# Kernel optimization log

Hardware: AMD Instinct MI355X
Metric: run time of the kernel (lower is better)

## Reference

```python
import jax, jax.numpy as jnp
import numpy as np

B, S, F = 4, 2048, 8
D, H, L, FF = 256, 8, 2, 1024
DH = D // H
NSK, NPAT = 2000, 64
DQ = D // 4  # pattern/feat sub-embedding width


def setup_inputs() -> dict:
    key = jax.random.key(0)
    ks = jax.random.split(key, 32)
    r = lambda i, shape: jax.random.normal(ks[i], shape, jnp.float32) * 0.02
    return {
        'interactions': jax.random.randint(ks[0], (B, S), 0, 2 * NSK),
        'patterns': jax.random.randint(ks[1], (B, S), 0, NPAT),
        'forget_features': jax.random.normal(ks[2], (B, S, F), jnp.float32),
        'inter_emb': r(3, (2 * NSK, D)),
        'pattern_emb': r(4, (NPAT, DQ)),
        'feat_W': r(5, (F, DQ)), 'feat_b': jnp.zeros((DQ,), jnp.float32),
        'in_W': r(6, (D + 2 * DQ, D)), 'in_b': jnp.zeros((D,), jnp.float32),
        'time_W': r(7, (1, D)), 'time_b': jnp.zeros((D,), jnp.float32),
        'pos_W': r(8, (1, D)), 'pos_b': jnp.zeros((D,), jnp.float32),
        'Wq': r(9, (L, D, H, DH)), 'bq': jnp.zeros((L, H, DH), jnp.float32),
        'Wk': r(10, (L, D, H, DH)), 'bk': jnp.zeros((L, H, DH), jnp.float32),
        'Wv': r(11, (L, D, H, DH)), 'bv': jnp.zeros((L, H, DH), jnp.float32),
        'Wo': r(12, (L, H, DH, D)), 'bo': jnp.zeros((L, D), jnp.float32),
        'kerple_p': jnp.full((L, H, 1, 1), 0.5, jnp.float32),
        'kerple_a': jnp.zeros((L, H, 1, 1), jnp.float32),
        'ln1_g': jnp.ones((L, D), jnp.float32), 'ln1_b': jnp.zeros((L, D), jnp.float32),
        'ln2_g': jnp.ones((L, D), jnp.float32), 'ln2_b': jnp.zeros((L, D), jnp.float32),
        'ffn_W1': r(13, (L, D, FF)), 'ffn_b1': jnp.zeros((L, FF), jnp.float32),
        'ffn_W2': r(14, (L, FF, D)), 'ffn_b2': jnp.zeros((L, D), jnp.float32),
        'out_W': r(15, (D, NSK)), 'out_b': jnp.zeros((NSK,), jnp.float32),
    }


def _ln(x, g, b, eps=1e-6):
    m = jnp.mean(x, -1, keepdims=True)
    v = jnp.mean(jnp.square(x - m), -1, keepdims=True)
    return g * (x - m) * jax.lax.rsqrt(v + eps) + b


def reference(interactions, patterns, forget_features, inter_emb, pattern_emb,
              feat_W, feat_b, in_W, in_b, time_W, time_b, pos_W, pos_b,
              Wq, bq, Wk, bk, Wv, bv, Wo, bo, kerple_p, kerple_a,
              ln1_g, ln1_b, ln2_g, ln2_b, ffn_W1, ffn_b1, ffn_W2, ffn_b2,
              out_W, out_b):
    inter_e = inter_emb[interactions]                      # [B,S,D]
    pat_e = pattern_emb[patterns]                          # [B,S,D/4]
    feat_e = forget_features @ feat_W + feat_b             # [B,S,D/4]
    x = jnp.concatenate([inter_e, pat_e, feat_e], -1) @ in_W + in_b  # [B,S,D]
    elapsed = forget_features[:, :, 0:1]
    time_enc = jnp.tanh(elapsed @ time_W + time_b)
    pos = jnp.arange(S, dtype=jnp.float32)[None, :, None] / jnp.float32(S)
    pos_enc = pos @ pos_W + pos_b
    x = x + time_enc + pos_enc

    positions = jnp.arange(S, dtype=jnp.float32)
    dist = jnp.maximum(positions[:, None] - positions[None, :], 0.0)  # [S,S]
    causal_bias = jnp.triu(jnp.full((S, S), -1e9, jnp.float32), 1)    # [S,S]
    inv_sqrt_dh = 1.0 / jnp.sqrt(jnp.float32(DH))

    for i in range(L):
        p = jax.nn.softplus(kerple_p[i])                   # [H,1,1]
        a = jax.nn.softplus(kerple_a[i])
        bias = causal_bias[None] - p * jnp.log1p(a * dist[None])  # [H,S,S]
        q = jnp.einsum('bsd,dhk->bshk', x, Wq[i]) + bq[i]
        k = jnp.einsum('bsd,dhk->bshk', x, Wk[i]) + bk[i]
        v = jnp.einsum('bsd,dhk->bshk', x, Wv[i]) + bv[i]
        scores = jnp.einsum('bshk,bthk->bhst', q, k) * inv_sqrt_dh + bias[None]
        attn = jax.nn.softmax(scores, axis=-1)
        o = jnp.einsum('bhst,bthk->bshk', attn, v)
        attn_out = jnp.einsum('bshk,hkd->bsd', o, Wo[i]) + bo[i]
        x = _ln(x + attn_out, ln1_g[i], ln1_b[i])
        h = jax.nn.gelu(x @ ffn_W1[i] + ffn_b1[i], approximate=False)
        ffn_out = h @ ffn_W2[i] + ffn_b2[i]
        x = _ln(x + ffn_out, ln2_g[i], ln2_b[i])
    return x @ out_W + out_b
```

## Files before the change

### kernel.cpp

```cpp
#include <hip/hip_runtime.h>
#include <math.h>

#define SEQ   2048
#define BATCH 4
#define NTOK  8192
#define DM    256
#define NHD   8
#define DHD   32
#define DFF   1024
#define NSKC  2000

typedef __attribute__((ext_vector_type(8))) short short8;
typedef __attribute__((ext_vector_type(4))) float f32x4;
typedef unsigned short ushort_t;

#define QPRE ((float)(0.17677669529663687 * 1.4426950408889634))

#define SPERM(i) (((i) & ~31) | (((i) & 15) << 1) | (((i) >> 4) & 1))

__device__ __forceinline__ ushort_t f2bf(float x) {
    union { float f; unsigned u; } c; c.f = x;
    unsigned r = c.u + 0x7FFFu + ((c.u >> 16) & 1u);
    return (ushort_t)(r >> 16);
}

#if __has_builtin(__builtin_amdgcn_cvt_pk_bf16_f32)
typedef __attribute__((ext_vector_type(2))) __bf16 bf16x2_t;
__device__ __forceinline__ unsigned pack_bf16(float a, float b) {
    bf16x2_t r = __builtin_amdgcn_cvt_pk_bf16_f32(a, b);
    union { bf16x2_t v; unsigned u; } c; c.v = r;
    return c.u;
}
#else
__device__ __forceinline__ unsigned pack_bf16(float a, float b) {
    return (unsigned)f2bf(a) | ((unsigned)f2bf(b) << 16);
}
#endif

#if __has_builtin(__builtin_amdgcn_exp2f)
__device__ __forceinline__ float fexp2(float x) { return __builtin_amdgcn_exp2f(x); }
#else
__device__ __forceinline__ float fexp2(float x) { return exp2f(x); }
#endif

__device__ __forceinline__ float bf2f(ushort_t x) {
    union { unsigned u; float f; } c; c.u = ((unsigned)x) << 16;
    return c.f;
}

__device__ __forceinline__ short8 mk_s8(unsigned a, unsigned b, unsigned c, unsigned d) {
    union { unsigned u[4]; short8 s; } t;
    t.u[0] = a; t.u[1] = b; t.u[2] = c; t.u[3] = d;
    return t.s;
}

struct ConvSeg { const float* src; ushort_t* dst; int K; int N; int ntx; int base; int kperm; };
struct ConvArgs { ConvSeg s[14]; };

__global__ __launch_bounds__(256) void convert_kernel(ConvArgs args) {
    int bid = blockIdx.x;
    int si = 0;
#pragma unroll
    for (int i = 1; i < 14; i++) if (bid >= args.s[i].base) si = i;
    ConvSeg sg = args.s[si];
    int local = bid - sg.base;
    int ty = local / sg.ntx;
    int tx = local - ty * sg.ntx;
    int n0 = tx * 32, k0 = ty * 32;
    __shared__ float T[32][33];
    int tid = threadIdx.x;
    int tn = tid & 31, tk4 = tid >> 5;
#pragma unroll
    for (int i = 0; i < 4; i++) {
        int kl = tk4 + i * 8;
        float v = 0.0f;
        if (n0 + tn < sg.N) v = sg.src[(size_t)(k0 + kl) * sg.N + n0 + tn];
        T[kl][tn] = v;
    }
    __syncthreads();
    int tk = tid & 31, tn4 = tid >> 5;
    int tks = sg.kperm ? (((tk & 15) << 1) | ((tk >> 4) & 1)) : tk;
#pragma unroll
    for (int i = 0; i < 4; i++) {
        int nl = tn4 + i * 8;
        sg.dst[(size_t)(n0 + nl) * sg.K + k0 + tks] = f2bf(T[tk][nl]);
    }
}

__global__ __launch_bounds__(384) void concat_kernel(
    const int* __restrict__ interactions, const int* __restrict__ patterns,
    const float* __restrict__ ff, const float* __restrict__ inter_emb,
    const float* __restrict__ pattern_emb, const float* __restrict__ feat_W,
    const float* __restrict__ feat_b, ushort_t* __restrict__ out)
{
    int tok = blockIdx.x;
    int j = threadIdx.x;
    float v;
    if (j < 256) {
        v = inter_emb[(size_t)interactions[tok] * 256 + j];
    } else if (j < 320) {
        v = pattern_emb[patterns[tok] * 64 + (j - 256)];
    } else {
        int c = j - 320;
        float acc = feat_b[c];
#pragma unroll
        for (int f = 0; f < 8; f++) acc += ff[tok * 8 + f] * feat_W[f * 64 + c];
        v = acc;
    }
    out[(size_t)tok * 384 + j] = f2bf(v);
}

__global__ __launch_bounds__(256) void ln_kernel(
    float* __restrict__ x, const ushort_t* __restrict__ r,
    const float* __restrict__ g, const float* __restrict__ b,
    ushort_t* __restrict__ xb)
{
    int tok = blockIdx.x;
    int d = threadIdx.x;
    int ds = SPERM(d);
    size_t row = (size_t)tok * DM;
    float v = x[row + d] + bf2f(r[row + ds]);
    float s1 = v, s2 = v * v;
#pragma unroll
    for (int off = 32; off > 0; off >>= 1) {
        s1 += __shfl_down(s1, off, 64);
        s2 += __shfl_down(s2, off, 64);
    }
    __shared__ float red1[4], red2[4];
    int wid = d >> 6, lane = d & 63;
    if (lane == 0) { red1[wid] = s1; red2[wid] = s2; }
    __syncthreads();
    s1 = red1[0] + red1[1] + red1[2] + red1[3];
    s2 = red2[0] + red2[1] + red2[2] + red2[3];
    float mean = s1 * (1.0f / 256.0f);
    float var = s2 * (1.0f / 256.0f) - mean * mean;
    float inv = rsqrtf(var + 1e-6f);
    float nv = g[d] * (v - mean) * inv + b[d];
    x[row + d] = nv;
    xb[row + ds] = f2bf(nv);
}

__global__ __launch_bounds__(256) void gemm64(
    const ushort_t* __restrict__ A, const ushort_t* __restrict__ Bt,
    int M, int N, int K, int mode,
    float* __restrict__ Cf, ushort_t* __restrict__ Cb,
    const float* __restrict__ b0,
    const float* __restrict__ ffg, const float* __restrict__ tW,
    const float* __restrict__ tb, const float* __restrict__ pW,
    const float* __restrict__ pb)
{
    __shared__ ushort_t As[2][64][40];
    __shared__ ushort_t Bs[2][64][40];
    int m0 = blockIdx.x * 64, n0 = blockIdx.y * 64;
    int tid = threadIdx.x;
    int wv = tid >> 6, lane = tid & 63;
    int quad = lane >> 4, l16 = lane & 15;
    int srow = tid >> 2, sc = (tid & 3) << 3;

    f32x4 acc[4];
#pragma unroll
    for (int j = 0; j < 4; j++) acc[j] = (f32x4){0.f, 0.f, 0.f, 0.f};

    uint4 pa = *(const uint4*)&A[(size_t)(m0 + srow) * K + sc];
    uint4 pbv = *(const uint4*)&Bt[(size_t)(n0 + srow) * K + sc];
    *(uint4*)&As[0][srow][sc] = pa;
    *(uint4*)&Bs[0][srow][sc] = pbv;

    int mrow = wv * 16;
    for (int k0 = 0; k0 < K; k0 += 32) {
        int cur = (k0 >> 5) & 1;
        __syncthreads();
        bool more = (k0 + 32 < K);
        if (more) {
            pa = *(const uint4*)&A[(size_t)(m0 + srow) * K + k0 + 32 + sc];
            pbv = *(const uint4*)&Bt[(size_t)(n0 + srow) * K + k0 + 32 + sc];
        }
        short8 af = *(const short8*)&As[cur][mrow + l16][quad * 8];
        short8 bf0 = *(const short8*)&Bs[cur][l16][quad * 8];
        short8 bf1 = *(const short8*)&Bs[cur][16 + l16][quad * 8];
        short8 bf2 = *(const short8*)&Bs[cur][32 + l16][quad * 8];
        short8 bf3 = *(const short8*)&Bs[cur][48 + l16][quad * 8];
        acc[0] = __builtin_amdgcn_mfma_f32_16x16x32_bf16(af, bf0, acc[0], 0, 0, 0);
        acc[1] = __builtin_amdgcn_mfma_f32_16x16x32_bf16(af, bf1, acc[1], 0, 0, 0);
        acc[2] = __builtin_amdgcn_mfma_f32_16x16x32_bf16(af, bf2, acc[2], 0, 0, 0);
        acc[3] = __builtin_amdgcn_mfma_f32_16x16x32_bf16(af, bf3, acc[3], 0, 0, 0);
        if (more) {
            *(uint4*)&As[cur ^ 1][srow][sc] = pa;
            *(uint4*)&Bs[cur ^ 1][srow][sc] = pbv;
        }
    }

#pragma unroll
    for (int r = 0; r < 4; r++) {
        int m = m0 + mrow + quad * 4 + r;
        if (mode == 4) {
            int s = m & (SEQ - 1);
            float el = ffg[m * 8];
            float pos = (float)s * (1.0f / (float)SEQ);
#pragma unroll
            for (int nt = 0; nt < 4; nt += 2) {
                int nlo = n0 + nt * 16 + l16;
                int nhi = nlo + 16;
                float v0 = acc[nt][r] + b0[nlo] + tanhf(el * tW[nlo] + tb[nlo]) + pos * pW[nlo] + pb[nlo];
                float v1 = acc[nt + 1][r] + b0[nhi] + tanhf(el * tW[nhi] + tb[nhi]) + pos * pW[nhi] + pb[nhi];
                Cf[(size_t)m * N + nlo] = v0;
                Cf[(size_t)m * N + nhi] = v1;
                *(unsigned*)&Cb[(size_t)m * N + n0 + nt * 16 + 2 * l16] = pack_bf16(v0, v1);
            }
        } else {
#pragma unroll
            for (int nt = 0; nt < 4; nt += 2) {
                int nlo = n0 + nt * 16 + l16;
                float v0 = acc[nt][r] + b0[nlo];
                float v1 = acc[nt + 1][r] + b0[nlo + 16];
                *(unsigned*)&Cb[(size_t)m * N + n0 + nt * 16 + 2 * l16] = pack_bf16(v0, v1);
            }
        }
    }
}

__global__ __launch_bounds__(256) void gemm_db(
    const ushort_t* __restrict__ A, const ushort_t* __restrict__ Bt,
    int M, int N, int K, int mode,
    ushort_t* __restrict__ Cb, ushort_t* __restrict__ Ck, ushort_t* __restrict__ Cv,
    const float* __restrict__ b0, const float* __restrict__ b1,
    const float* __restrict__ b2)
{
    __shared__ ushort_t As[2][128][40];
    __shared__ ushort_t Bs[2][64][40];
    int m0 = blockIdx.x * 128, n0 = blockIdx.y * 64;
    int tid = threadIdx.x;
    int wv = tid >> 6, lane = tid & 63;
    int quad = lane >> 4, l16 = lane & 15;
    int srow = tid >> 2, sc = (tid & 3) << 3;

    f32x4 acc[2][4];
#pragma unroll
    for (int i = 0; i < 2; i++)
#pragma unroll
        for (int j = 0; j < 4; j++) acc[i][j] = (f32x4){0.f, 0.f, 0.f, 0.f};

    uint4 pa0 = *(const uint4*)&A[(size_t)(m0 + srow) * K + sc];
    uint4 pa1 = *(const uint4*)&A[(size_t)(m0 + 64 + srow) * K + sc];
    uint4 pbb = *(const uint4*)&Bt[(size_t)(n0 + srow) * K + sc];
    *(uint4*)&As[0][srow][sc] = pa0;
    *(uint4*)&As[0][64 + srow][sc] = pa1;
    *(uint4*)&Bs[0][srow][sc] = pbb;

    int msub = wv * 32;
    for (int k0 = 0; k0 < K; k0 += 32) {
        int cur = (k0 >> 5) & 1;
        __syncthreads();
        bool more = (k0 + 32 < K);
        if (more) {
            pa0 = *(const uint4*)&A[(size_t)(m0 + srow) * K + k0 + 32 + sc];
            pa1 = *(const uint4*)&A[(size_t)(m0 + 64 + srow) * K + k0 + 32 + sc];
            pbb = *(const uint4*)&Bt[(size_t)(n0 + srow) * K + k0 + 32 + sc];
        }
        short8 af0 = *(const short8*)&As[cur][msub + l16][quad * 8];
        short8 af1 = *(const short8*)&As[cur][msub + 16 + l16][quad * 8];
        short8 bf0 = *(const short8*)&Bs[cur][l16][quad * 8];
        short8 bf1 = *(const short8*)&Bs[cur][16 + l16][quad * 8];
        short8 bf2 = *(const short8*)&Bs[cur][32 + l16][quad * 8];
        short8 bf3 = *(const short8*)&Bs[cur][48 + l16][quad * 8];
        acc[0][0] = __builtin_amdgcn_mfma_f32_16x16x32_bf16(af0, bf0, acc[0][0], 0, 0, 0);
        acc[0][1] = __builtin_amdgcn_mfma_f32_16x16x32_bf16(af0, bf1, acc[0][1], 0, 0, 0);
        acc[0][2] = __builtin_amdgcn_mfma_f32_16x16x32_bf16(af0, bf2, acc[0][2], 0, 0, 0);
        acc[0][3] = __builtin_amdgcn_mfma_f32_16x16x32_bf16(af0, bf3, acc[0][3], 0, 0, 0);
        acc[1][0] = __builtin_amdgcn_mfma_f32_16x16x32_bf16(af1, bf0, acc[1][0], 0, 0, 0);
        acc[1][1] = __builtin_amdgcn_mfma_f32_16x16x32_bf16(af1, bf1, acc[1][1], 0, 0, 0);
        acc[1][2] = __builtin_amdgcn_mfma_f32_16x16x32_bf16(af1, bf2, acc[1][2], 0, 0, 0);
        acc[1][3] = __builtin_amdgcn_mfma_f32_16x16x32_bf16(af1, bf3, acc[1][3], 0, 0, 0);
        if (more) {
            *(uint4*)&As[cur ^ 1][srow][sc] = pa0;
            *(uint4*)&As[cur ^ 1][64 + srow][sc] = pa1;
            *(uint4*)&Bs[cur ^ 1][srow][sc] = pbb;
        }
    }

#pragma unroll
    for (int mt = 0; mt < 2; mt++) {
#pragma unroll
        for (int nt = 0; nt < 4; nt += 2) {
            int nlo = n0 + nt * 16 + l16;
#pragma unroll
            for (int r = 0; r < 4; r++) {
                int m = m0 + msub + mt * 16 + quad * 4 + r;
                float vlo = acc[mt][nt][r];
                float vhi = acc[mt][nt + 1][r];
                if (mode == 1) {
                    float t0 = vlo + b0[nlo];
                    float t1 = vhi + b0[nlo + 16];
                    t0 = 0.5f * t0 * (1.0f + erff(t0 * 0.70710678118654752f));
                    t1 = 0.5f * t1 * (1.0f + erff(t1 * 0.70710678118654752f));
                    *(unsigned*)&Cb[(size_t)m * N + n0 + nt * 16 + 2 * l16] = pack_bf16(t0, t1);
                } else {
                    int which = nlo >> 8, idx = nlo & 255;
                    int hh = idx >> 5;
                    int s = m & (SEQ - 1), b = m >> 11;
                    if (which == 0) {
                        float q0 = (vlo + b0[idx]) * QPRE;
                        float q1 = (vhi + b0[idx + 16]) * QPRE;
                        *(unsigned*)&Cb[(((size_t)(b * NHD + hh)) * SEQ + s) * DHD + 2 * l16] = pack_bf16(q0, q1);
                    } else if (which == 1) {
                        float k0v = vlo + b1[idx];
                        float k1v = vhi + b1[idx + 16];
                        *(unsigned*)&Ck[(((size_t)(b * NHD + hh)) * SEQ + s) * DHD + 2 * l16] = pack_bf16(k0v, k1v);
                    } else {
                        Cv[(((size_t)(b * NHD + hh)) * DHD + l16) * SEQ + s] = f2bf(vlo + b2[idx]);
                        Cv[(((size_t)(b * NHD + hh)) * DHD + l16 + 16) * SEQ + s] = f2bf(vhi + b2[idx + 16]);
                    }
                }
            }
        }
    }
}

__global__ __launch_bounds__(256) void gemm_out(
    const ushort_t* __restrict__ A, const ushort_t* __restrict__ Bt,
    int M, int N, int K,
    float* __restrict__ Cf, const float* __restrict__ b0, int Nreal)
{
    __shared__ ushort_t As[2][128][40];
    __shared__ ushort_t Bs[2][128][40];
    int m0 = blockIdx.x * 128, n0 = blockIdx.y * 128;
    int tid = threadIdx.x;
    int wv = tid >> 6, lane = tid & 63;
    int quad = lane >> 4, l16 = lane & 15;
    int wm = (wv >> 1) * 64, wn = (wv & 1) * 64;
    int srow = tid >> 1, sc = (tid & 1) << 4;

    f32x4 acc[4][4];
#pragma unroll
    for (int i = 0; i < 4; i++)
#pragma unroll
        for (int j = 0; j < 4; j++) acc[i][j] = (f32x4){0.f, 0.f, 0.f, 0.f};

    uint4 pa0 = *(const uint4*)&A[(size_t)(m0 + srow) * K + sc];
    uint4 pa1 = *(const uint4*)&A[(size_t)(m0 + srow) * K + sc + 8];
    uint4 pb0 = *(const uint4*)&Bt[(size_t)(n0 + srow) * K + sc];
    uint4 pb1 = *(const uint4*)&Bt[(size_t)(n0 + srow) * K + sc + 8];
    *(uint4*)&As[0][srow][sc] = pa0;
    *(uint4*)&As[0][srow][sc + 8] = pa1;
    *(uint4*)&Bs[0][srow][sc] = pb0;
    *(uint4*)&Bs[0][srow][sc + 8] = pb1;

    for (int k0 = 0; k0 < K; k0 += 32) {
        int cur = (k0 >> 5) & 1;
        __syncthreads();
        bool more = (k0 + 32 < K);
        if (more) {
            pa0 = *(const uint4*)&A[(size_t)(m0 + srow) * K + k0 + 32 + sc];
            pa1 = *(const uint4*)&A[(size_t)(m0 + srow) * K + k0 + 32 + sc + 8];
            pb0 = *(const uint4*)&Bt[(size_t)(n0 + srow) * K + k0 + 32 + sc];
            pb1 = *(const uint4*)&Bt[(size_t)(n0 + srow) * K + k0 + 32 + sc + 8];
        }
        short8 af[4], bf[4];
#pragma unroll
        for (int i = 0; i < 4; i++) {
            af[i] = *(const short8*)&As[cur][wm + i * 16 + l16][quad * 8];
            bf[i] = *(const short8*)&Bs[cur][wn + i * 16 + l16][quad * 8];
        }
#pragma unroll
        for (int i = 0; i < 4; i++)
#pragma unroll
            for (int j = 0; j < 4; j++)
                acc[i][j] = __builtin_amdgcn_mfma_f32_16x16x32_bf16(af[i], bf[j], acc[i][j], 0, 0, 0);
        if (more) {
            *(uint4*)&As[cur ^ 1][srow][sc] = pa0;
            *(uint4*)&As[cur ^ 1][srow][sc + 8] = pa1;
            *(uint4*)&Bs[cur ^ 1][srow][sc] = pb0;
            *(uint4*)&Bs[cur ^ 1][srow][sc + 8] = pb1;
        }
    }

#pragma unroll
    for (int i = 0; i < 4; i++) {
#pragma unroll
        for (int j = 0; j < 4; j++) {
            int n = n0 + wn + j * 16 + l16;
            if (n < Nreal) {
#pragma unroll
                for (int r = 0; r < 4; r++) {
                    int m = m0 + wm + i * 16 + quad * 4 + r;
                    Cf[(size_t)m * Nreal + n] = acc[i][j][r] + b0[n];
                }
            }
        }
    }
}

__global__ __launch_bounds__(256) void attn_mfma(
    const ushort_t* __restrict__ qb, const ushort_t* __restrict__ kb,
    const ushort_t* __restrict__ vtb, const float* __restrict__ kp,
    const float* __restrict__ ka, ushort_t* __restrict__ ob)
{
    int gid = blockIdx.x;
    int hb = ((gid >> 9) << 3) | (gid & 7);
    int pj = (gid >> 3) & 63;
    int b = hb >> 3, h = hb & 7;

    int tid = threadIdx.x, wv = tid >> 6, lane = tid & 63;
    int quad = lane >> 4, l16 = lane & 15;

    __shared__ float tabs[2112];
    __shared__ __align__(16) float ShA[2560];
    __shared__ float LsB[128];

    float p = log1pf(__expf(kp[h]));
    float a = log1pf(__expf(ka[h]));
    for (int i = tid; i < 2112; i += 256) {
        float w = 0.0f;
        if (i >= 64) w = fexp2(-p * __log2f(fmaf(a, (float)(i - 64), 1.0f)));
        tabs[i] = w;
    }
    __syncthreads();

    int bh = b * NHD + h;
    const ushort_t* Qh = qb + (size_t)bh * SEQ * DHD;
    const ushort_t* Kh = kb + (size_t)bh * SEQ * DHD;
    const ushort_t* Vh = vtb + (size_t)bh * DHD * SEQ;

    int tlo = pj, thi = 127 - pj;
    int qlo0 = tlo * 16, qhi0 = thi * 16;

    short8 qfl = *(const short8*)&Qh[(qlo0 + l16) * DHD + quad * 8];
    short8 qfh = *(const short8*)&Qh[(qhi0 + l16) * DHD + quad * 8];
    f32x4 ol0 = (f32x4){0.f,0.f,0.f,0.f}, ol1 = (f32x4){0.f,0.f,0.f,0.f};
    f32x4 oh0 = (f32x4){0.f,0.f,0.f,0.f}, oh1 = (f32x4){0.f,0.f,0.f,0.f};
    float lsh_s = 0.f, lsl_s = 0.f;

    int nch_hi = (thi + 2) >> 1;
    int nch_lo = (tlo + 2) >> 1;
    int krow = ((l16 >> 2) << 3) | (l16 & 3);
    int tb_h = qhi0 + l16 + 64 - 8 * quad;
    int tb_l = qlo0 + l16 + 64 - 8 * quad;

    int ch = wv;
    short8 kf0n, kf1n;
    {
        int k0 = ch * 32;
        kf0n = *(const short8*)&Kh[(k0 + krow) * DHD + quad * 8];
        kf1n = *(const short8*)&Kh[(k0 + 4 + krow) * DHD + quad * 8];
    }

    for (; ch < nch_hi; ch += 4) {
        int k0 = ch * 32;
        short8 kf0 = kf0n, kf1 = kf1n;
        short8 vf0 = *(const short8*)&Vh[l16 * SEQ + k0 + quad * 8];
        short8 vf1 = *(const short8*)&Vh[(16 + l16) * SEQ + k0 + quad * 8];
        int chn = ch + 4;
        if (chn < nch_hi) {
            int kn = chn * 32;
            kf0n = *(const short8*)&Kh[(kn + krow) * DHD + quad * 8];
            kf1n = *(const short8*)&Kh[(kn + 4 + krow) * DHD + quad * 8];
        }
        f32x4 z = (f32x4){0.f,0.f,0.f,0.f};

        f32x4 s0 = __builtin_amdgcn_mfma_f32_16x16x32_bf16(kf0, qfh, z, 0, 0, 0);
        f32x4 s1 = __builtin_amdgcn_mfma_f32_16x16x32_bf16(kf1, qfh, z, 0, 0, 0);
        {
            const float* tp = &tabs[tb_h - k0];
            float e0 = fexp2(s0[0]) * tp[0];
            float e1 = fexp2(s0[1]) * tp[-1];
            float e2 = fexp2(s0[2]) * tp[-2];
            float e3 = fexp2(s0[3]) * tp[-3];
            unsigned p0 = pack_bf16(e0, e1);
            unsigned p1 = pack_bf16(e2, e3);
            float f0 = fexp2(s1[0]) * tp[-4];
            float f1 = fexp2(s1[1]) * tp[-5];
            float f2 = fexp2(s1[2]) * tp[-6];
            float f3 = fexp2(s1[3]) * tp[-7];
            unsigned p2 = pack_bf16(f0, f1);
            unsigned p3 = pack_bf16(f2, f3);
            lsh_s += ((e0 + e1) + (e2 + e3)) + ((f0 + f1) + (f2 + f3));
            short8 pf = mk_s8(p0, p1, p2, p3);
            oh0 = __builtin_amdgcn_mfma_f32_16x16x32_bf16(pf, vf0, oh0, 0, 0, 0);
            oh1 = __builtin_amdgcn_mfma_f32_16x16x32_bf16(pf, vf1, oh1, 0, 0, 0);
        }
        if (ch < nch_lo) {
            f32x4 t0 = __builtin_amdgcn_mfma_f32_16x16x32_bf16(kf0, qfl, z, 0, 0, 0);
            f32x4 t1 = __builtin_amdgcn_mfma_f32_16x16x32_bf16(kf1, qfl, z, 0, 0, 0);
            const float* tq = &tabs[tb_l - k0];
            float e0 = fexp2(t0[0]) * tq[0];
            float e1 = fexp2(t0[1]) * tq[-1];
            float e2 = fexp2(t0[2]) * tq[-2];
            float e3 = fexp2(t0[3]) * tq[-3];
            unsigned p0 = pack_bf16(e0, e1);
            unsigned p1 = pack_bf16(e2, e3);
            float f0 = fexp2(t1[0]) * tq[-4];
            float f1 = fexp2(t1[1]) * tq[-5];
            float f2 = fexp2(t1[2]) * tq[-6];
            float f3 = fexp2(t1[3]) * tq[-7];
            unsigned p2 = pack_bf16(f0, f1);
            unsigned p3 = pack_bf16(f2, f3);
            lsl_s += ((e0 + e1) + (e2 + e3)) + ((f0 + f1) + (f2 + f3));
            short8 pf = mk_s8(p0, p1, p2, p3);
            ol0 = __builtin_amdgcn_mfma_f32_16x16x32_bf16(pf, vf0, ol0, 0, 0, 0);
            ol1 = __builtin_amdgcn_mfma_f32_16x16x32_bf16(pf, vf1, ol1, 0, 0, 0);
        }
    }

    lsh_s += __shfl_xor(lsh_s, 16, 64);
    lsh_s += __shfl_xor(lsh_s, 32, 64);
    lsl_s += __shfl_xor(lsl_s, 16, 64);
    lsl_s += __shfl_xor(lsl_s, 32, 64);
    if (lane < 16) {
        LsB[wv * 32 + lane] = lsh_s;
        LsB[wv * 32 + 16 + lane] = lsl_s;
    }

    float* cp = &ShA[((wv >> 1) * 64 + lane) * 20];
    if (wv & 1) {
        *(float4*)&cp[0]  = (float4){oh0[0], oh0[1], oh0[2], oh0[3]};
        *(float4*)&cp[4]  = (float4){oh1[0], oh1[1], oh1[2], oh1[3]};
        *(float4*)&cp[8]  = (float4){ol0[0], ol0[1], ol0[2], ol0[3]};
        *(float4*)&cp[12] = (float4){ol1[0], ol1[1], ol1[2], ol1[3]};
    }
    __syncthreads();
    if (!(wv & 1)) {
#pragma unroll
        for (int i = 0; i < 4; i++) {
            oh0[i] += cp[i];      oh1[i] += cp[4 + i];
            ol0[i] += cp[8 + i];  ol1[i] += cp[12 + i];
        }
    }
    __syncthreads();
    if (wv == 2) {
        float* c0 = &ShA[lane * 20];
        *(float4*)&c0[0]  = (float4){oh0[0], oh0[1], oh0[2], oh0[3]};
        *(float4*)&c0[4]  = (float4){oh1[0], oh1[1], oh1[2], oh1[3]};
        *(float4*)&c0[8]  = (float4){ol0[0], ol0[1], ol0[2], ol0[3]};
        *(float4*)&c0[12] = (float4){ol1[0], ol1[1], ol1[2], ol1[3]};
    }
    __syncthreads();
    if (wv == 0) {
        const float* c0 = &ShA[lane * 20];
#pragma unroll
        for (int i = 0; i < 4; i++) {
            oh0[i] += c0[i];      oh1[i] += c0[4 + i];
            ol0[i] += c0[8 + i];  ol1[i] += c0[12 + i];
        }
        int qr = quad * 4;
        int qsrh = qhi0 + qr, qsrl = qlo0 + qr;
#pragma unroll
        for (int r = 0; r < 4; r++) {
            float dh = (LsB[qr + r] + LsB[32 + qr + r]) + (LsB[64 + qr + r] + LsB[96 + qr + r]);
            float dl = (LsB[16 + qr + r] + LsB[48 + qr + r]) + (LsB[80 + qr + r] + LsB[112 + qr + r]);
            float rh = 1.0f / dh;
            float rl = 1.0f / dl;
            size_t bh_ = ((size_t)(b * SEQ + qsrh + r)) * DM + h * DHD;
            size_t bl_ = ((size_t)(b * SEQ + qsrl + r)) * DM + h * DHD;
            *(unsigned*)&ob[bh_ + 2 * l16] = pack_bf16(oh0[r] * rh, oh1[r] * rh);
            *(unsigned*)&ob[bl_ + 2 * l16] = pack_bf16(ol0[r] * rl, ol1[r] * rl);
        }
    }
}

extern "C" void kernel_launch(void* const* d_in, const int* in_sizes, int n_in,
                              void* d_out, int out_size, void* d_ws, size_t ws_size,
                              hipStream_t stream) {
    const int*   interactions = (const int*)d_in[0];
    const int*   patterns     = (const int*)d_in[1];
    const float* ff           = (const float*)d_in[2];
    const float* inter_emb    = (const float*)d_in[3];
    const float* pattern_emb  = (const float*)d_in[4];
    const float* feat_W       = (const float*)d_in[5];
    const float* feat_b       = (const float*)d_in[6];
    const float* in_W         = (const float*)d_in[7];
    const float* in_b         = (const float*)d_in[8];
    const float* time_W       = (const float*)d_in[9];
    const float* time_b       = (const float*)d_in[10];
    const float* pos_W        = (const float*)d_in[11];
    const float* pos_b        = (const float*)d_in[12];
    const float* Wq           = (const float*)d_in[13];
    const float* bq           = (const float*)d_in[14];
    const float* Wk           = (const float*)d_in[15];
    const float* bk           = (const float*)d_in[16];
    const float* Wv           = (const float*)d_in[17];
    const float* bv           = (const float*)d_in[18];
    const float* Wo           = (const float*)d_in[19];
    const float* bo           = (const float*)d_in[20];
    const float* kerple_p     = (const float*)d_in[21];
    const float* kerple_a     = (const float*)d_in[22];
    const float* ln1_g        = (const float*)d_in[23];
    const float* ln1_b        = (const float*)d_in[24];
    const float* ln2_g        = (const float*)d_in[25];
    const float* ln2_b        = (const float*)d_in[26];
    const float* ffn_W1       = (const float*)d_in[27];
    const float* ffn_b1       = (const float*)d_in[28];
    const float* ffn_W2       = (const float*)d_in[29];
    const float* ffn_b2       = (const float*)d_in[30];
    const float* out_W        = (const float*)d_in[31];
    const float* out_b        = (const float*)d_in[32];
    float* out = (float*)d_out;

    char* wsb = (char*)d_ws;
    const size_t MB = 1024 * 1024;
    float*    x    = (float*)(wsb + 0);
    ushort_t* tmpb = (ushort_t*)(wsb + 8  * MB);
    ushort_t* xb   = (ushort_t*)(wsb + 16 * MB);
    ushort_t* qbuf = (ushort_t*)(wsb + 20 * MB);
    ushort_t* kbuf = (ushort_t*)(wsb + 24 * MB);
    ushort_t* vtbf = (ushort_t*)(wsb + 28 * MB);
    ushort_t* shrd = (ushort_t*)(wsb + 32 * MB);
    ushort_t* cbuf = shrd;
    ushort_t* o_bf = shrd;
    ushort_t* h_bf = shrd;
    char* wp = wsb + 48 * MB;
    ushort_t* inWt  = (ushort_t*)wp;  wp += 256  * 384 * 2;
    ushort_t* qkvWt = (ushort_t*)wp;  wp += 2 * 768 * 256 * 2;
    ushort_t* WoT   = (ushort_t*)wp;  wp += 2 * 256 * 256 * 2;
    ushort_t* W1T   = (ushort_t*)wp;  wp += 2 * 1024 * 256 * 2;
    ushort_t* W2T   = (ushort_t*)wp;  wp += 2 * 256 * 1024 * 2;
    ushort_t* outWt = (ushort_t*)wp;  wp += 2048 * 256 * 2;

    ConvArgs ca;
    int D2 = 256 * 256;
    int base = 0, ib = 0;
    auto addseg = [&](const float* src, ushort_t* dst, int K, int N, int Npad, int kp) {
        ca.s[ib].src = src; ca.s[ib].dst = dst; ca.s[ib].K = K; ca.s[ib].N = N;
        ca.s[ib].ntx = Npad / 32; ca.s[ib].base = base; ca.s[ib].kperm = kp;
        base += (Npad / 32) * (K / 32); ib++;
    };
    addseg(in_W,            inWt,           384,  256,  256,  0);
    addseg(Wq,              qkvWt,          256,  256,  256,  1);
    addseg(Wk,              qkvWt + 1 * D2, 256,  256,  256,  1);
    addseg(Wv,              qkvWt + 2 * D2, 256,  256,  256,  1);
    addseg(Wq + D2,         qkvWt + 3 * D2, 256,  256,  256,  1);
    addseg(Wk + D2,         qkvWt + 4 * D2, 256,  256,  256,  1);
    addseg(Wv + D2,         qkvWt + 5 * D2, 256,  256,  256,  1);
    addseg(Wo,              WoT,            256,  256,  256,  1);
    addseg(Wo + D2,         WoT + D2,       256,  256,  256,  1);
    addseg(ffn_W1,          W1T,            256,  1024, 1024, 1);
    addseg(ffn_W1 + 4 * D2, W1T + 4 * D2,   256,  1024, 1024, 1);
    addseg(ffn_W2,          W2T,            1024, 256,  256,  1);
    addseg(ffn_W2 + 4 * D2, W2T + 4 * D2,   1024, 256,  256,  1);
    addseg(out_W,           outWt,          256,  2000, 2048, 1);
    convert_kernel<<<base, 256, 0, stream>>>(ca);

    concat_kernel<<<NTOK, 384, 0, stream>>>(interactions, patterns, ff,
                                            inter_emb, pattern_emb, feat_W, feat_b, cbuf);
    gemm64<<<dim3(128, 4), 256, 0, stream>>>(cbuf, inWt, NTOK, 256, 384, 4,
                                             x, xb, in_b, ff, time_W, time_b, pos_W, pos_b);

    for (int l = 0; l < 2; l++) {
        gemm_db<<<dim3(64, 12), 256, 0, stream>>>(
            xb, qkvWt + (size_t)l * 768 * 256, NTOK, 768, 256, 2,
            qbuf, kbuf, vtbf, bq + l * 256, bk + l * 256, bv + l * 256);
        attn_mfma<<<2048, 256, 0, stream>>>(
            qbuf, kbuf, vtbf, kerple_p + l * NHD, kerple_a + l * NHD, o_bf);
        gemm64<<<dim3(128, 4), 256, 0, stream>>>(
            o_bf, WoT + (size_t)l * D2, NTOK, 256, 256, 5,
            nullptr, tmpb, bo + l * 256, nullptr, nullptr, nullptr, nullptr, nullptr);
        ln_kernel<<<NTOK, 256, 0, stream>>>(x, tmpb, ln1_g + l * 256, ln1_b + l * 256, xb);
        gemm_db<<<dim3(64, 16), 256, 0, stream>>>(
            xb, W1T + (size_t)l * 4 * D2, NTOK, 1024, 256, 1,
            h_bf, nullptr, nullptr, ffn_b1 + l * 1024, nullptr, nullptr);
        gemm64<<<dim3(128, 4), 256, 0, stream>>>(
            h_bf, W2T + (size_t)l * 4 * D2, NTOK, 256, 1024, 5,
            nullptr, tmpb, ffn_b2 + l * 256, nullptr, nullptr, nullptr, nullptr, nullptr);
        ln_kernel<<<NTOK, 256, 0, stream>>>(x, tmpb, ln2_g + l * 256, ln2_b + l * 256, xb);
    }

    gemm_out<<<dim3(64, 16), 256, 0, stream>>>(
        xb, outWt, NTOK, 2048, 256, out, out_b, NSKC);
}
```

Measured before the change: 403.0 us.

## Fuse output-projection and FFN-down GEMMs with residual add and LayerNorm

Adds a gemm_ln kernel where each block computes a full 16x256 output row tile, so the residual add, bias and LayerNorm statistics can be done in the GEMM epilogue through a small shared-memory reduction. This removes the separate ln_kernel launches and the bf16 temporary buffer round trip, four times per forward pass. In exchange, each block re-reads the whole 256-wide weight slice for only 16 rows, which lowers arithmetic intensity and may hurt the K=1024 FFN-down GEMM. The residual path also now stays in fp32 instead of being rounded to bf16 in between.

```diff
diff --git a/kernel.cpp b/kernel.cpp
--- a/kernel.cpp
+++ b/kernel.cpp
@@ -110,36 +110,6 @@
     out[(size_t)tok * 384 + j] = f2bf(v);
 }
 
-__global__ __launch_bounds__(256) void ln_kernel(
-    float* __restrict__ x, const ushort_t* __restrict__ r,
-    const float* __restrict__ g, const float* __restrict__ b,
-    ushort_t* __restrict__ xb)
-{
-    int tok = blockIdx.x;
-    int d = threadIdx.x;
-    int ds = SPERM(d);
-    size_t row = (size_t)tok * DM;
-    float v = x[row + d] + bf2f(r[row + ds]);
-    float s1 = v, s2 = v * v;
-#pragma unroll
-    for (int off = 32; off > 0; off >>= 1) {
-        s1 += __shfl_down(s1, off, 64);
-        s2 += __shfl_down(s2, off, 64);
-    }
-    __shared__ float red1[4], red2[4];
-    int wid = d >> 6, lane = d & 63;
-    if (lane == 0) { red1[wid] = s1; red2[wid] = s2; }
-    __syncthreads();
-    s1 = red1[0] + red1[1] + red1[2] + red1[3];
-    s2 = red2[0] + red2[1] + red2[2] + red2[3];
-    float mean = s1 * (1.0f / 256.0f);
-    float var = s2 * (1.0f / 256.0f) - mean * mean;
-    float inv = rsqrtf(var + 1e-6f);
-    float nv = g[d] * (v - mean) * inv + b[d];
-    x[row + d] = nv;
-    xb[row + ds] = f2bf(nv);
-}
-
 __global__ __launch_bounds__(256) void gemm64(
     const ushort_t* __restrict__ A, const ushort_t* __restrict__ Bt,
     int M, int N, int K, int mode,
@@ -216,6 +186,135 @@
                 *(unsigned*)&Cb[(size_t)m * N + n0 + nt * 16 + 2 * l16] = pack_bf16(v0, v1);
             }
         }
+    }
+}
+
+__global__ __launch_bounds__(256) void gemm_ln(
+    const ushort_t* __restrict__ A, const ushort_t* __restrict__ Bt,
+    int K,
+    const float* __restrict__ b0,
+    float* __restrict__ x,
+    const float* __restrict__ g, const float* __restrict__ bln,
+    ushort_t* __restrict__ xb)
+{
+    __shared__ ushort_t As[2][16][40];
+    __shared__ ushort_t Bs[2][256][40];
+    __shared__ float LnS[4][16][2];
+    int m0 = blockIdx.x * 16;
+    int tid = threadIdx.x;
+    int wv = tid >> 6, lane = tid & 63;
+    int quad = lane >> 4, l16 = lane & 15;
+    int wn = wv * 64;
+
+    f32x4 acc[4];
+#pragma unroll
+    for (int j = 0; j < 4; j++) acc[j] = (f32x4){0.f, 0.f, 0.f, 0.f};
+
+    int ar = tid >> 2, ac = (tid & 3) << 3;
+
+    float xo[4][4];
+#pragma unroll
+    for (int nt = 0; nt < 4; nt++) {
+        int col = wn + nt * 16 + l16;
+#pragma unroll
+        for (int r = 0; r < 4; r++)
+            xo[nt][r] = x[(size_t)(m0 + quad * 4 + r) * DM + col];
+    }
+
+    uint4 pb[4];
+#pragma unroll
+    for (int q = 0; q < 4; q++)
+        pb[q] = *(const uint4*)&Bt[(size_t)tid * K + q * 8];
+    uint4 pa;
+    if (tid < 64) pa = *(const uint4*)&A[(size_t)(m0 + ar) * K + ac];
+#pragma unroll
+    for (int q = 0; q < 4; q++)
+        *(uint4*)&Bs[0][tid][q * 8] = pb[q];
+    if (tid < 64) *(uint4*)&As[0][ar][ac] = pa;
+
+    for (int k0 = 0; k0 < K; k0 += 32) {
+        int cur = (k0 >> 5) & 1;
+        __syncthreads();
+        bool more = (k0 + 32 < K);
+        if (more) {
+#pragma unroll
+            for (int q = 0; q < 4; q++)
+                pb[q] = *(const uint4*)&Bt[(size_t)tid * K + k0 + 32 + q * 8];
+            if (tid < 64) pa = *(const uint4*)&A[(size_t)(m0 + ar) * K + k0 + 32 + ac];
+        }
+        short8 af = *(const short8*)&As[cur][l16][quad * 8];
+        short8 bf0 = *(const short8*)&Bs[cur][wn + l16][quad * 8];
+        short8 bf1 = *(const short8*)&Bs[cur][wn + 16 + l16][quad * 8];
+        short8 bf2 = *(const short8*)&Bs[cur][wn + 32 + l16][quad * 8];
+        short8 bf3 = *(const short8*)&Bs[cur][wn + 48 + l16][quad * 8];
+        acc[0] = __builtin_amdgcn_mfma_f32_16x16x32_bf16(af, bf0, acc[0], 0, 0, 0);
+        acc[1] = __builtin_amdgcn_mfma_f32_16x16x32_bf16(af, bf1, acc[1], 0, 0, 0);
+        acc[2] = __builtin_amdgcn_mfma_f32_16x16x32_bf16(af, bf2, acc[2], 0, 0, 0);
+        acc[3] = __builtin_amdgcn_mfma_f32_16x16x32_bf16(af, bf3, acc[3], 0, 0, 0);
+        if (more) {
+#pragma unroll
+            for (int q = 0; q < 4; q++)
+                *(uint4*)&Bs[cur ^ 1][tid][q * 8] = pb[q];
+            if (tid < 64) *(uint4*)&As[cur ^ 1][ar][ac] = pa;
+        }
+    }
+
+    float vv[4][4];
+    float s1[4] = {0.f, 0.f, 0.f, 0.f}, s2[4] = {0.f, 0.f, 0.f, 0.f};
+#pragma unroll
+    for (int nt = 0; nt < 4; nt++) {
+        int col = wn + nt * 16 + l16;
+        float bb = b0[col];
+#pragma unroll
+        for (int r = 0; r < 4; r++) {
+            float t = acc[nt][r] + bb + xo[nt][r];
+            vv[nt][r] = t;
+            s1[r] += t;
+            s2[r] += t * t;
+        }
+    }
+#pragma unroll
+    for (int r = 0; r < 4; r++) {
+#pragma unroll
+        for (int off = 1; off < 16; off <<= 1) {
+            s1[r] += __shfl_xor(s1[r], off, 16);
+            s2[r] += __shfl_xor(s2[r], off, 16);
+        }
+    }
+    if (l16 == 0) {
+#pragma unroll
+        for (int r = 0; r < 4; r++) {
+            LnS[wv][quad * 4 + r][0] = s1[r];
+            LnS[wv][quad * 4 + r][1] = s2[r];
+        }
+    }
+    __syncthreads();
+
+    float gg[4], bb2[4];
+#pragma unroll
+    for (int nt = 0; nt < 4; nt++) {
+        int col = wn + nt * 16 + l16;
+        gg[nt] = g[col];
+        bb2[nt] = bln[col];
+    }
+#pragma unroll
+    for (int r = 0; r < 4; r++) {
+        int row = quad * 4 + r;
+        float t1 = (LnS[0][row][0] + LnS[1][row][0]) + (LnS[2][row][0] + LnS[3][row][0]);
+        float t2 = (LnS[0][row][1] + LnS[1][row][1]) + (LnS[2][row][1] + LnS[3][row][1]);
+        float mean = t1 * (1.0f / 256.0f);
+        float var = t2 * (1.0f / 256.0f) - mean * mean;
+        float inv = rsqrtf(var + 1e-6f);
+        float nv[4];
+#pragma unroll
+        for (int nt = 0; nt < 4; nt++) {
+            int col = wn + nt * 16 + l16;
+            nv[nt] = gg[nt] * (vv[nt][r] - mean) * inv + bb2[nt];
+            x[(size_t)(m0 + row) * DM + col] = nv[nt];
+        }
+        size_t rb = (size_t)(m0 + row) * DM;
+        *(unsigned*)&xb[rb + wn + 2 * l16]      = pack_bf16(nv[0], nv[1]);
+        *(unsigned*)&xb[rb + wn + 32 + 2 * l16] = pack_bf16(nv[2], nv[3]);
     }
 }
 
@@ -598,7 +697,6 @@
     char* wsb = (char*)d_ws;
     const size_t MB = 1024 * 1024;
     float*    x    = (float*)(wsb + 0);
-    ushort_t* tmpb = (ushort_t*)(wsb + 8  * MB);
     ushort_t* xb   = (ushort_t*)(wsb + 16 * MB);
     ushort_t* qbuf = (ushort_t*)(wsb + 20 * MB);
     ushort_t* kbuf = (ushort_t*)(wsb + 24 * MB);
@@ -650,17 +748,15 @@
             qbuf, kbuf, vtbf, bq + l * 256, bk + l * 256, bv + l * 256);
         attn_mfma<<<2048, 256, 0, stream>>>(
             qbuf, kbuf, vtbf, kerple_p + l * NHD, kerple_a + l * NHD, o_bf);
-        gemm64<<<dim3(128, 4), 256, 0, stream>>>(
-            o_bf, WoT + (size_t)l * D2, NTOK, 256, 256, 5,
-            nullptr, tmpb, bo + l * 256, nullptr, nullptr, nullptr, nullptr, nullptr);
-        ln_kernel<<<NTOK, 256, 0, stream>>>(x, tmpb, ln1_g + l * 256, ln1_b + l * 256, xb);
+        gemm_ln<<<NTOK / 16, 256, 0, stream>>>(
+            o_bf, WoT + (size_t)l * D2, 256,
+            bo + l * 256, x, ln1_g + l * 256, ln1_b + l * 256, xb);
         gemm_db<<<dim3(64, 16), 256, 0, stream>>>(
             xb, W1T + (size_t)l * 4 * D2, NTOK, 1024, 256, 1,
             h_bf, nullptr, nullptr, ffn_b1 + l * 1024, nullptr, nullptr);
-        gemm64<<<dim3(128, 4), 256, 0, stream>>>(
-            h_bf, W2T + (size_t)l * 4 * D2, NTOK, 256, 1024, 5,
-            nullptr, tmpb, ffn_b2 + l * 256, nullptr, nullptr, nullptr, nullptr, nullptr);
-        ln_kernel<<<NTOK, 256, 0, stream>>>(x, tmpb, ln2_g + l * 256, ln2_b + l * 256, xb);
+        gemm_ln<<<NTOK / 16, 256, 0, stream>>>(
+            h_bf, W2T + (size_t)l * 4 * D2, 1024,
+            ffn_b2 + l * 256, x, ln2_g + l * 256, ln2_b + l * 256, xb);
     }
 
     gemm_out<<<dim3(64, 16), 256, 0, stream>>>(
```

Result: slower. 549.5 us (+36.4%).
